# Performance work log

Hardware: AMD Instinct MI355X
Metric: run time of the kernel (lower is better)

Reference implementation:

```python
import jax, jax.numpy as jnp
import numpy as np

N_NODES = 50000
N_EDGES = 800000
D_FEAT = 64          # per-node feature dim
HIDDEN = 128         # fc1 output dim; fc1 input = 2*D_FEAT


def setup_inputs() -> dict:
    key = jax.random.key(0)
    k1, k2, k3 = jax.random.split(key, 3)
    x = jax.random.normal(k1, (N_NODES, D_FEAT), dtype=jnp.float32)
    edge_index = jax.random.randint(k2, (2, N_EDGES), 0, N_NODES, dtype=jnp.int64)
    # fc1: Linear(2*D_FEAT, HIDDEN); torch Linear weight is [out, in]
    W = jax.random.normal(k3, (HIDDEN, 2 * D_FEAT), dtype=jnp.float32) * (1.0 / np.sqrt(2 * D_FEAT))
    b = jnp.zeros((HIDDEN,), dtype=jnp.float32)
    return {"x": x, "edge_index": edge_index, "W": W, "b": b}


def reference(x, edge_index, W, b):
    # Gather source-node features along edges, sum-scatter to destinations.
    src, dst = edge_index[0], edge_index[1]
    gathered = x[src]  # [E, D_FEAT] -- dominant memory traffic
    neigh = jax.ops.segment_sum(gathered, dst, num_segments=x.shape[0])  # [N, D_FEAT]
    # Concat self features with aggregated neighbor features, then Linear+ReLU.
    h = jnp.concatenate([x, neigh], axis=-1)          # [N, 2*D_FEAT]
    out = jax.nn.relu(h @ W.T + b)                    # [N, HIDDEN]
    return out
```

## Files before the change

kernel.cpp:

```cpp
#include <hip/hip_runtime.h>

#define N_NODES 50000
#define N_EDGES 800000
#define DFEAT 64
#define HID 128
#define NBKT 782
#define NSEG 391
#define SEGW 16
#define CAP_S 1536
#define NSTR 66

#define XB2 1563
#define WB2 8
#define EB2 391

typedef __bf16 bf16x8 __attribute__((ext_vector_type(8)));
typedef float f32x4 __attribute__((ext_vector_type(4)));

__device__ inline unsigned short f2bf(float f) {
  unsigned u = __float_as_uint(f);
  return (unsigned short)((u + 0x7FFFu + ((u >> 16) & 1u)) >> 16);
}
__device__ inline float bf2f(unsigned short h) {
  return __uint_as_float(((unsigned)h) << 16);
}

__global__ __launch_bounds__(512) void k_prep(const float* __restrict__ x,
                                              const float* __restrict__ W,
                                              const int* __restrict__ ei,
                                              unsigned short* __restrict__ xb,
                                              unsigned short* __restrict__ Wb,
                                              unsigned int* __restrict__ coarse) {
  int bid = blockIdx.x;
  const int tid = threadIdx.x;
  if (bid < XB2) {
    int t = bid * 512 + tid;
    if (t < N_NODES * DFEAT / 4) {
      float4 v = *(const float4*)&x[t * 4];
      ushort4 o = {f2bf(v.x), f2bf(v.y), f2bf(v.z), f2bf(v.w)};
      *(ushort4*)&xb[t * 4] = o;
    }
    return;
  }
  bid -= XB2;
  if (bid < WB2) {
    int t = bid * 512 + tid;
    float4 v = *(const float4*)&W[t * 4];
    ushort4 o = {f2bf(v.x), f2bf(v.y), f2bf(v.z), f2bf(v.w)};
    *(ushort4*)&Wb[t * 4] = o;
    return;
  }
  bid -= WB2;
  __shared__ int lcnt[NBKT];
  for (int i = tid; i < NBKT; i += 512) lcnt[i] = 0;
  __syncthreads();

  int e0 = (bid * 512 + tid) * 4;
  if (e0 < N_EDGES) {
    int4 s4 = *(const int4*)&ei[e0];
    int4 d4 = *(const int4*)&ei[N_EDGES + e0];
    int ss[4] = {s4.x, s4.y, s4.z, s4.w};
    int dd[4] = {d4.x, d4.y, d4.z, d4.w};
#pragma unroll
    for (int i = 0; i < 4; ++i) {
      int bkt = dd[i] >> 6;
      int rank = atomicAdd(&lcnt[bkt], 1);
      if (rank < SEGW - 1)
        coarse[(size_t)bkt * (NSEG * SEGW) + bid * SEGW + 1 + rank] =
            ((unsigned)dd[i] << 16) | (unsigned)ss[i];
    }
  }
  __syncthreads();
  for (int i = tid; i < NBKT; i += 512) {
    int c = lcnt[i];
    coarse[(size_t)i * (NSEG * SEGW) + bid * SEGW] =
        (unsigned)(c < SEGW - 1 ? c : SEGW - 1);
  }
}

__global__ __launch_bounds__(1024) void k_gnn(const unsigned short* __restrict__ xb,
                                              const unsigned short* __restrict__ Wb,
                                              const unsigned int* __restrict__ coarse,
                                              const float* __restrict__ bv,
                                              float* __restrict__ out) {
  __shared__ unsigned int q[CAP_S];
  __shared__ unsigned int sq[CAP_S];
  __shared__ unsigned int ns_u[32 * NSTR];
  __shared__ int scnt[NSEG];
  __shared__ int lcnt[64];
  __shared__ int lbase[65];
  __shared__ int qn;

  const int tid = threadIdx.x;
  const int b = blockIdx.x;
  const int nb = b * 64;
  const unsigned int* base = coarse + (size_t)b * (NSEG * SEGW);

  if (tid < 64) lcnt[tid] = 0;
  if (tid == 0) qn = 0;
  for (int i = tid; i < NSEG; i += 1024) {
    int c = (int)base[i * SEGW];
    scnt[i] = c < SEGW - 1 ? c : SEGW - 1;
  }
  __syncthreads();

  const int NU4 = NSEG * SEGW / 4;
  for (int i = tid; i < NU4; i += 1024) {
    uint4 w = ((const uint4*)base)[i];
    int seg = i >> 2;
    int wi = (i & 3) * 4;
    int cnt = scnt[seg];
    unsigned e[4] = {w.x, w.y, w.z, w.w};
#pragma unroll
    for (int k = 0; k < 4; ++k) {
      int widx = wi + k;
      if (widx >= 1 && widx <= cnt) {
        int pos = atomicAdd(&qn, 1);
        if (pos < CAP_S) q[pos] = e[k] & 0x003fffffu;
      }
    }
  }
  __syncthreads();

  int cnt = qn < CAP_S ? qn : CAP_S;

  int myrank[2], myidx[2], nloc = 0;
  for (int i = tid; i < cnt; i += 1024) {
    int rel = (int)(q[i] >> 16);
    myrank[nloc] = atomicAdd(&lcnt[rel], 1);
    myidx[nloc] = i;
    ++nloc;
  }
  __syncthreads();
  if (tid < 64) {
    int v = lcnt[tid];
    int inc = v;
#pragma unroll
    for (int o = 1; o < 64; o <<= 1) {
      int u = __shfl_up(inc, o);
      if (tid >= o) inc += u;
    }
    lbase[tid] = inc - v;
    if (tid == 63) lbase[64] = inc;
  }
  __syncthreads();
  for (int k = 0; k < nloc; ++k) {
    unsigned e = q[myidx[k]];
    sq[lbase[e >> 16] + myrank[k]] = e;
  }
  __syncthreads();

  const int wave = tid >> 6;
  const int lane = tid & 63;
  const int eslot = lane >> 4;
  const int c = lane & 15;
  const uint2* xu2 = (const uint2*)xb;

#pragma unroll
  for (int i2 = 0; i2 < 4; ++i2) {
    int n = wave * 4 + i2;
    int beg = lbase[n], end = lbase[n + 1];
    float f0 = 0.f, f1 = 0.f, f2 = 0.f, f3 = 0.f;
    float g0 = 0.f, g1 = 0.f, g2 = 0.f, g3 = 0.f;
    int j = beg + eslot;
    for (; j + 4 < end; j += 8) {
      unsigned e0 = sq[j], e1 = sq[j + 4];
      uint2 v0 = xu2[(e0 & 0xffffu) * 16 + c];
      uint2 v1 = xu2[(e1 & 0xffffu) * 16 + c];
      f0 += bf2f((unsigned short)(v0.x & 0xffffu)); f1 += bf2f((unsigned short)(v0.x >> 16));
      f2 += bf2f((unsigned short)(v0.y & 0xffffu)); f3 += bf2f((unsigned short)(v0.y >> 16));
      g0 += bf2f((unsigned short)(v1.x & 0xffffu)); g1 += bf2f((unsigned short)(v1.x >> 16));
      g2 += bf2f((unsigned short)(v1.y & 0xffffu)); g3 += bf2f((unsigned short)(v1.y >> 16));
    }
    for (; j < end; j += 4) {
      unsigned e = sq[j];
      uint2 v = xu2[(e & 0xffffu) * 16 + c];
      f0 += bf2f((unsigned short)(v.x & 0xffffu)); f1 += bf2f((unsigned short)(v.x >> 16));
      f2 += bf2f((unsigned short)(v.y & 0xffffu)); f3 += bf2f((unsigned short)(v.y >> 16));
    }
    f0 += g0; f1 += g1; f2 += g2; f3 += g3;
    f0 += __shfl_xor(f0, 16); f0 += __shfl_xor(f0, 32);
    f1 += __shfl_xor(f1, 16); f1 += __shfl_xor(f1, 32);
    f2 += __shfl_xor(f2, 16); f2 += __shfl_xor(f2, 32);
    f3 += __shfl_xor(f3, 16); f3 += __shfl_xor(f3, 32);
    if (eslot == 0) {
      ns_u[(2 * c) * NSTR + n] = (unsigned)f2bf(f0) | ((unsigned)f2bf(f1) << 16);
      ns_u[(2 * c + 1) * NSTR + n] = (unsigned)f2bf(f2) | ((unsigned)f2bf(f3) << 16);
    }
  }
  __syncthreads();

  const int g = wave & 3;
  const int o = wave >> 2;
  const int l15 = lane & 15;
  const int quad = lane >> 4;
  const int node0 = nb + g * 16;

  int anode = node0 + l15;
  if (anode >= N_NODES) anode = N_NODES - 1;
  const unsigned short* hx = xb + (size_t)anode * DFEAT;

  bf16x8 fa0 = *(const bf16x8*)(hx + quad * 8);
  bf16x8 fa1 = *(const bf16x8*)(hx + 32 + quad * 8);
  bf16x8 fa2, fa3;
  {
    int m = g * 16 + l15;
    union { unsigned u[4]; bf16x8 v; } c2, c3;
#pragma unroll
    for (int i = 0; i < 4; ++i) {
      c2.u[i] = ns_u[(quad * 4 + i) * NSTR + m];
      c3.u[i] = ns_u[(16 + quad * 4 + i) * NSTR + m];
    }
    fa2 = c2.v;
    fa3 = c3.v;
  }

  f32x4 accr[2];
#pragma unroll
  for (int t = 0; t < 2; ++t) accr[t] = (f32x4){0.f, 0.f, 0.f, 0.f};

#pragma unroll
  for (int t = 0; t < 2; ++t) {
    int nt = o * 2 + t;
    const unsigned short* wr = Wb + (size_t)(nt * 16 + l15) * (2 * DFEAT) + quad * 8;
    bf16x8 b0 = *(const bf16x8*)(wr);
    bf16x8 b1 = *(const bf16x8*)(wr + 32);
    bf16x8 b2 = *(const bf16x8*)(wr + 64);
    bf16x8 b3 = *(const bf16x8*)(wr + 96);
    accr[t] = __builtin_amdgcn_mfma_f32_16x16x32_bf16(fa0, b0, accr[t], 0, 0, 0);
    accr[t] = __builtin_amdgcn_mfma_f32_16x16x32_bf16(fa1, b1, accr[t], 0, 0, 0);
    accr[t] = __builtin_amdgcn_mfma_f32_16x16x32_bf16(fa2, b2, accr[t], 0, 0, 0);
    accr[t] = __builtin_amdgcn_mfma_f32_16x16x32_bf16(fa3, b3, accr[t], 0, 0, 0);
  }

#pragma unroll
  for (int t = 0; t < 2; ++t) {
    int nt = o * 2 + t;
    float bias = bv[nt * 16 + l15];
#pragma unroll
    for (int r = 0; r < 4; ++r) {
      int node = node0 + quad * 4 + r;
      if (node < N_NODES) {
        float v = accr[t][r] + bias;
        out[(size_t)node * HID + nt * 16 + l15] = v > 0.f ? v : 0.f;
      }
    }
  }
}

extern "C" void kernel_launch(void* const* d_in, const int* in_sizes, int n_in,
                              void* d_out, int out_size, void* d_ws, size_t ws_size,
                              hipStream_t stream) {
  const float* x = (const float*)d_in[0];
  const int* ei = (const int*)d_in[1];
  const float* W = (const float*)d_in[2];
  const float* b = (const float*)d_in[3];
  float* out = (float*)d_out;

  char* ws = (char*)d_ws;
  unsigned int* coarse = (unsigned int*)ws;   ws += (size_t)NBKT * NSEG * SEGW * 4;
  unsigned short* xb   = (unsigned short*)ws; ws += (size_t)N_NODES * DFEAT * 2;
  unsigned short* Wb   = (unsigned short*)ws; ws += (size_t)HID * 2 * DFEAT * 2;

  k_prep<<<XB2 + WB2 + EB2, 512, 0, stream>>>(x, W, ei, xb, Wb, coarse);
  k_gnn<<<NBKT, 1024, 0, stream>>>(xb, Wb, coarse, b, out);
}
```

Measured before the change: 127.4 us.

## Replace per-block counting sort with LDS float atomics for neighbor aggregation

The local counting sort of edges by destination node (rank atomics, prefix scan, scatter, plus two barriers) is removed. Each 16-lane group now takes edges straight from the unsorted queue, gathers the source row, and accumulates into a 64x66 fp32 shared-memory tile with LDS float atomicAdd. The block-wide sync and sort overhead go away and all 64 lanes stay busy regardless of per-node degree imbalance. In exchange there are four LDS atomics per lane per edge, possible contention on hot destinations, and non-deterministic summation order.

```diff
diff --git a/kernel.cpp b/kernel.cpp
--- a/kernel.cpp
+++ b/kernel.cpp
@@ -8,7 +8,6 @@
 #define NSEG 391
 #define SEGW 16
 #define CAP_S 1536
-#define NSTR 66
 
 #define XB2 1563
 #define WB2 8
@@ -84,11 +83,8 @@
                                               const float* __restrict__ bv,
                                               float* __restrict__ out) {
   __shared__ unsigned int q[CAP_S];
-  __shared__ unsigned int sq[CAP_S];
-  __shared__ unsigned int ns_u[32 * NSTR];
+  __shared__ float ns[64][66];
   __shared__ int scnt[NSEG];
-  __shared__ int lcnt[64];
-  __shared__ int lbase[65];
   __shared__ int qn;
 
   const int tid = threadIdx.x;
@@ -96,7 +92,7 @@
   const int nb = b * 64;
   const unsigned int* base = coarse + (size_t)b * (NSEG * SEGW);
 
-  if (tid < 64) lcnt[tid] = 0;
+  for (int i = tid; i < 64 * 66; i += 1024) ((float*)ns)[i] = 0.f;
   if (tid == 0) qn = 0;
   for (int i = tid; i < NSEG; i += 1024) {
     int c = (int)base[i * SEGW];
@@ -109,12 +105,12 @@
     uint4 w = ((const uint4*)base)[i];
     int seg = i >> 2;
     int wi = (i & 3) * 4;
-    int cnt = scnt[seg];
+    int cw = scnt[seg];
     unsigned e[4] = {w.x, w.y, w.z, w.w};
 #pragma unroll
     for (int k = 0; k < 4; ++k) {
       int widx = wi + k;
-      if (widx >= 1 && widx <= cnt) {
+      if (widx >= 1 && widx <= cw) {
         int pos = atomicAdd(&qn, 1);
         if (pos < CAP_S) q[pos] = e[k] & 0x003fffffu;
       }
@@ -124,72 +120,53 @@
 
   int cnt = qn < CAP_S ? qn : CAP_S;
 
-  int myrank[2], myidx[2], nloc = 0;
-  for (int i = tid; i < cnt; i += 1024) {
-    int rel = (int)(q[i] >> 16);
-    myrank[nloc] = atomicAdd(&lcnt[rel], 1);
-    myidx[nloc] = i;
-    ++nloc;
-  }
-  __syncthreads();
-  if (tid < 64) {
-    int v = lcnt[tid];
-    int inc = v;
-#pragma unroll
-    for (int o = 1; o < 64; o <<= 1) {
-      int u = __shfl_up(inc, o);
-      if (tid >= o) inc += u;
-    }
-    lbase[tid] = inc - v;
-    if (tid == 63) lbase[64] = inc;
-  }
-  __syncthreads();
-  for (int k = 0; k < nloc; ++k) {
-    unsigned e = q[myidx[k]];
-    sq[lbase[e >> 16] + myrank[k]] = e;
-  }
+  const int et = tid >> 4;
+  const int ch = tid & 15;
+  const uint2* xu2 = (const uint2*)xb;
+
+#define ACC(E, V)                                                        \
+  {                                                                      \
+    float* p = &ns[(E) >> 16][ch * 4];                                   \
+    atomicAdd(p + 0, bf2f((unsigned short)((V).x & 0xffffu)));           \
+    atomicAdd(p + 1, bf2f((unsigned short)((V).x >> 16)));               \
+    atomicAdd(p + 2, bf2f((unsigned short)((V).y & 0xffffu)));           \
+    atomicAdd(p + 3, bf2f((unsigned short)((V).y >> 16)));               \
+  }
+
+  const int fr = cnt >> 6;
+  int r = 0;
+  for (; r + 4 <= fr; r += 4) {
+    unsigned e0 = q[(r + 0) * 64 + et];
+    unsigned e1 = q[(r + 1) * 64 + et];
+    unsigned e2 = q[(r + 2) * 64 + et];
+    unsigned e3 = q[(r + 3) * 64 + et];
+    uint2 v0 = xu2[(size_t)(e0 & 0xffffu) * 16 + ch];
+    uint2 v1 = xu2[(size_t)(e1 & 0xffffu) * 16 + ch];
+    uint2 v2 = xu2[(size_t)(e2 & 0xffffu) * 16 + ch];
+    uint2 v3 = xu2[(size_t)(e3 & 0xffffu) * 16 + ch];
+    ACC(e0, v0);
+    ACC(e1, v1);
+    ACC(e2, v2);
+    ACC(e3, v3);
+  }
+  for (; r < fr; ++r) {
+    unsigned e = q[r * 64 + et];
+    uint2 v = xu2[(size_t)(e & 0xffffu) * 16 + ch];
+    ACC(e, v);
+  }
+  {
+    int idx = fr * 64 + et;
+    if (idx < cnt) {
+      unsigned e = q[idx];
+      uint2 v = xu2[(size_t)(e & 0xffffu) * 16 + ch];
+      ACC(e, v);
+    }
+  }
+#undef ACC
   __syncthreads();
 
   const int wave = tid >> 6;
   const int lane = tid & 63;
-  const int eslot = lane >> 4;
-  const int c = lane & 15;
-  const uint2* xu2 = (const uint2*)xb;
-
-#pragma unroll
-  for (int i2 = 0; i2 < 4; ++i2) {
-    int n = wave * 4 + i2;
-    int beg = lbase[n], end = lbase[n + 1];
-    float f0 = 0.f, f1 = 0.f, f2 = 0.f, f3 = 0.f;
-    float g0 = 0.f, g1 = 0.f, g2 = 0.f, g3 = 0.f;
-    int j = beg + eslot;
-    for (; j + 4 < end; j += 8) {
-      unsigned e0 = sq[j], e1 = sq[j + 4];
-      uint2 v0 = xu2[(e0 & 0xffffu) * 16 + c];
-      uint2 v1 = xu2[(e1 & 0xffffu) * 16 + c];
-      f0 += bf2f((unsigned short)(v0.x & 0xffffu)); f1 += bf2f((unsigned short)(v0.x >> 16));
-      f2 += bf2f((unsigned short)(v0.y & 0xffffu)); f3 += bf2f((unsigned short)(v0.y >> 16));
-      g0 += bf2f((unsigned short)(v1.x & 0xffffu)); g1 += bf2f((unsigned short)(v1.x >> 16));
-      g2 += bf2f((unsigned short)(v1.y & 0xffffu)); g3 += bf2f((unsigned short)(v1.y >> 16));
-    }
-    for (; j < end; j += 4) {
-      unsigned e = sq[j];
-      uint2 v = xu2[(e & 0xffffu) * 16 + c];
-      f0 += bf2f((unsigned short)(v.x & 0xffffu)); f1 += bf2f((unsigned short)(v.x >> 16));
-      f2 += bf2f((unsigned short)(v.y & 0xffffu)); f3 += bf2f((unsigned short)(v.y >> 16));
-    }
-    f0 += g0; f1 += g1; f2 += g2; f3 += g3;
-    f0 += __shfl_xor(f0, 16); f0 += __shfl_xor(f0, 32);
-    f1 += __shfl_xor(f1, 16); f1 += __shfl_xor(f1, 32);
-    f2 += __shfl_xor(f2, 16); f2 += __shfl_xor(f2, 32);
-    f3 += __shfl_xor(f3, 16); f3 += __shfl_xor(f3, 32);
-    if (eslot == 0) {
-      ns_u[(2 * c) * NSTR + n] = (unsigned)f2bf(f0) | ((unsigned)f2bf(f1) << 16);
-      ns_u[(2 * c + 1) * NSTR + n] = (unsigned)f2bf(f2) | ((unsigned)f2bf(f3) << 16);
-    }
-  }
-  __syncthreads();
-
   const int g = wave & 3;
   const int o = wave >> 2;
   const int l15 = lane & 15;
@@ -205,11 +182,11 @@
   bf16x8 fa2, fa3;
   {
     int m = g * 16 + l15;
-    union { unsigned u[4]; bf16x8 v; } c2, c3;
-#pragma unroll
-    for (int i = 0; i < 4; ++i) {
-      c2.u[i] = ns_u[(quad * 4 + i) * NSTR + m];
-      c3.u[i] = ns_u[(16 + quad * 4 + i) * NSTR + m];
+    union { unsigned short s[8]; bf16x8 v; } c2, c3;
+#pragma unroll
+    for (int i = 0; i < 8; ++i) {
+      c2.s[i] = f2bf(ns[m][quad * 8 + i]);
+      c3.s[i] = f2bf(ns[m][32 + quad * 8 + i]);
     }
     fa2 = c2.v;
     fa3 = c3.v;
@@ -238,10 +215,10 @@
     int nt = o * 2 + t;
     float bias = bv[nt * 16 + l15];
 #pragma unroll
-    for (int r = 0; r < 4; ++r) {
-      int node = node0 + quad * 4 + r;
+    for (int r2 = 0; r2 < 4; ++r2) {
+      int node = node0 + quad * 4 + r2;
       if (node < N_NODES) {
-        float v = accr[t][r] + bias;
+        float v = accr[t][r2] + bias;
         out[(size_t)node * HID + nt * 16 + l15] = v > 0.f ? v : 0.f;
       }
     }
```

Result: slower. 446.4 us (+250.3%).
